# Optimization experiments

Measured on AMD Instinct MI355X. Metric: run time of the kernel, lower is better.

The kernel has to match this reference:

```python
import jax, jax.numpy as jnp
import numpy as np

T, D, E, K = 8192, 7168, 256, 8
G, LG = 8, 4  # n_expert_groups, n_limited_groups
ROUTE_SCALE = 2.5


def setup_inputs() -> dict:
    key = jax.random.key(0)
    k1, k2, k3 = jax.random.split(key, 3)
    x = jax.random.normal(k1, (T, D), dtype=jnp.float32)
    W = jax.random.normal(k2, (E, D), dtype=jnp.float32) * (1.0 / np.sqrt(D))
    bias = jax.random.normal(k3, (E,), dtype=jnp.float32) * 0.01
    return {"x": x, "W": W, "bias": bias}


def reference(x, W, bias):
    # linear scorer: [T, E]
    logits = jnp.einsum("td,ed->te", x, W)
    original_scores = jax.nn.sigmoid(logits)
    scores = original_scores + bias  # bias only affects routing, not weights

    # group selection: reshape [T, G, E//G]; group score = sum of top-2 (bias path)
    scores_g = scores.reshape(T, G, E // G)
    group_scores = jax.lax.top_k(scores_g, 2)[0].sum(axis=-1)  # [T, G]
    _, gidx = jax.lax.top_k(group_scores, LG)  # [T, LG]
    keep = jnp.any(jnp.arange(G)[None, None, :] == gidx[:, :, None], axis=1)  # [T, G]
    scores_masked = jnp.where(keep[:, :, None], scores_g, -jnp.inf).reshape(T, E)

    # final top-k experts
    _, indices = jax.lax.top_k(scores_masked, K)  # [T, K] int32
    weights = jnp.take_along_axis(original_scores, indices, axis=1)  # [T, K]
    weights = weights / weights.sum(axis=-1, keepdims=True)  # sigmoid normalization
    weights = weights * ROUTE_SCALE
    weights = weights.astype(x.dtype)

    # per-expert token counts (indices unique per row, so scatter(1)+sum == histogram)
    counts = jnp.zeros((E,), dtype=jnp.int32).at[indices.reshape(-1)].add(1)
    return weights, indices.astype(jnp.int64), counts
```

## Files before the change

### kernel.cpp

```cpp
#include <hip/hip_runtime.h>
#include <math.h>
#include <stdint.h>

#define T_TOK 8192
#define D_DIM 7168
#define E_EXP 256
#define K_SEL 8
#define G_GRP 8
#define LG_GRP 4
#define ROUTE_SCALE 2.5f

#define BM 64
#define BN 128
#define BK 64
#define NKT (D_DIM / BK)
#define SCALE_LO 2048.0f
#define INV_SCALE (1.0f / 2048.0f)

typedef _Float16 half_t;
typedef _Float16 half8 __attribute__((ext_vector_type(8)));
typedef float f32x4 __attribute__((ext_vector_type(4)));

#define WF_HALVES_PER_H (2 * 112 * 16 * 512)

__device__ __forceinline__ void load_lds16(const void* g, void* l) {
    __builtin_amdgcn_global_load_lds(
        (const __attribute__((address_space(1))) uint32_t*)g,
        (__attribute__((address_space(3))) uint32_t*)l, 16, 0, 0);
}

__global__ __launch_bounds__(256)
void convert_W_kernel(const float* __restrict__ W, half_t* __restrict__ Wf) {
    const int u = blockIdx.x * 256 + threadIdx.x;
    const int slot = u & 63;
    const int ks   = (u >> 6) & 1;
    const int p    = (u >> 7) & 7;
    const int t2   = u >> 10;
    const int kt   = t2 % 112;
    const int nb   = t2 / 112;
    const int e = nb * 128 + p * 16 + (slot & 15);
    const int k = kt * 64 + ks * 32 + (slot >> 4) * 8;

    const float* src = W + (size_t)e * D_DIM + k;
    float4 v0 = *(const float4*)src;
    float4 v1 = *(const float4*)(src + 4);
    float f[8] = {v0.x, v0.y, v0.z, v0.w, v1.x, v1.y, v1.z, v1.w};
    half8 hi, lo;
    #pragma unroll
    for (int j = 0; j < 8; j++) {
        const half_t h = (half_t)f[j];
        hi[j] = h;
        lo[j] = (half_t)((f[j] - (float)h) * SCALE_LO);
    }
    *(half8*)&Wf[(size_t)u * 8] = hi;
    *(half8*)&Wf[(size_t)WF_HALVES_PER_H + (size_t)u * 8] = lo;
}

__global__ __launch_bounds__(256, 3)
void gemm_logits_f16split(const float* __restrict__ x,
                          const half_t* __restrict__ Wf,
                          float* __restrict__ planes,
                          int nsplit) {
    __shared__ __align__(16) half_t Ah[4 * 2 * 64 * 8];
    __shared__ __align__(16) half_t Al[4 * 2 * 64 * 8];
    __shared__ __align__(16) half_t Bbuf[2][16][512];

    const int tid = threadIdx.x;
    const int bid = blockIdx.x;
    const int nmod  = 2 * nsplit;
    const int g     = bid % nmod;
    const int j     = bid / nmod;
    const int nb    = g & 1;
    const int split = g >> 1;
    const int row0 = j * BM;

    int ks0, kt_len;
    if (nsplit == 3) { ks0 = split * 38 - (split == 2 ? 1 : 0);
                       kt_len = split ? 37 : 38; }
    else             { ks0 = split * (NKT / nsplit);
                       kt_len = NKT / nsplit; }

    const float* __restrict__ xA = x + (size_t)row0 * D_DIM;
    float* __restrict__ plane = planes + (size_t)split * T_TOK * E_EXP;

    const int wave = tid >> 6, lane = tid & 63;
    const int q = lane >> 4;
    const int mp0 = (wave >> 1) * 2;
    const int np0 = (wave & 1) * 4;

    const half_t* __restrict__ wfl = Wf + ((size_t)(2 + nb) * 112) * 16 * 512
                                        + (size_t)lane * 8;

    float4 pa[2][2];

    auto load_A = [&](int kt) {
        const int kbase = kt * BK;
        #pragma unroll
        for (int i = 0; i < 2; i++) {
            const int u = i * 256 + tid;
            const int r = u >> 3, k8 = u & 7;
            const float* p = xA + (size_t)r * D_DIM + kbase + k8 * 8;
            pa[i][0] = *(const float4*)p;
            pa[i][1] = *(const float4*)(p + 4);
        }
    };

    auto stage_A = [&]() {
        #pragma unroll
        for (int i = 0; i < 2; i++) {
            const int u = i * 256 + tid;
            const int r = u >> 3, k8 = u & 7;
            float f[8] = {pa[i][0].x, pa[i][0].y, pa[i][0].z, pa[i][0].w,
                          pa[i][1].x, pa[i][1].y, pa[i][1].z, pa[i][1].w};
            half8 hi, lo;
            #pragma unroll
            for (int jj = 0; jj < 8; jj++) {
                const half_t h = (half_t)f[jj];
                hi[jj] = h;
                lo[jj] = (half_t)((f[jj] - (float)h) * SCALE_LO);
            }
            const int m = r & 15, qq = k8 & 3, kss = k8 >> 2;
            const int slot = (m + 16 * qq) ^ k8;
            const int off = (((r >> 4) * 2 + kss) * 64 + slot) * 8;
            *(half8*)&Ah[off] = hi;
            *(half8*)&Al[off] = lo;
        }
    };

    auto issue_B = [&](int tt) {
        const int kt = ks0 + tt;
        half_t* bb = &Bbuf[tt & 1][0][0];
        #pragma unroll
        for (int i = 0; i < 4; i++) {
            const int sl = i * 4 + wave;
            const half_t* src = Wf +
                ((size_t)(nb * 112 + kt) * 16 + sl) * 512 + lane * 8;
            load_lds16(src, bb + sl * 512);
        }
    };

    f32x4 ach[2][4] = {}, acc[2][4] = {};

    auto compute = [&](int tt, bool pref) {
        const int kt = ks0 + tt;
        const half_t* bb = &Bbuf[tt & 1][0][0];

        half8 bl[4][2];
        const size_t ktoff = (size_t)kt * (16 * 512);
        #pragma unroll
        for (int ni = 0; ni < 4; ni++)
            #pragma unroll
            for (int ks = 0; ks < 2; ks++) {
                const int s32 = (np0 + ni) * 2 + ks;
                bl[ni][ks] = *(const half8*)(wfl + ktoff + (size_t)s32 * 512);
            }
        if (pref) {
            issue_B(tt + 1);
            load_A(ks0 + tt + 1);
        }
        #pragma unroll
        for (int ks = 0; ks < 2; ks++) {
            const int slot = lane ^ ((ks << 2) | q);
            half8 ah[2], al[2], bh[4];
            #pragma unroll
            for (int mi = 0; mi < 2; mi++) {
                const int off = (((mp0 + mi) * 2 + ks) * 64 + slot) * 8;
                ah[mi] = *(const half8*)&Ah[off];
                al[mi] = *(const half8*)&Al[off];
            }
            #pragma unroll
            for (int ni = 0; ni < 4; ni++) {
                const int s32 = (np0 + ni) * 2 + ks;
                bh[ni] = *(const half8*)&bb[s32 * 512 + lane * 8];
            }
            #pragma unroll
            for (int mi = 0; mi < 2; mi++)
                #pragma unroll
                for (int ni = 0; ni < 4; ni++) {
                    ach[mi][ni] = __builtin_amdgcn_mfma_f32_16x16x32_f16(ah[mi], bh[ni], ach[mi][ni], 0, 0, 0);
                    acc[mi][ni] = __builtin_amdgcn_mfma_f32_16x16x32_f16(ah[mi], bl[ni][ks], acc[mi][ni], 0, 0, 0);
                    acc[mi][ni] = __builtin_amdgcn_mfma_f32_16x16x32_f16(al[mi], bh[ni], acc[mi][ni], 0, 0, 0);
                }
        }
    };

    issue_B(0);
    load_A(ks0);

    #pragma unroll 1
    for (int tt = 0; tt < kt_len; tt++) {
        __syncthreads();
        stage_A();
        __syncthreads();
        compute(tt, tt + 1 < kt_len);
    }

    const int col0 = nb * BN;
    #pragma unroll
    for (int mi = 0; mi < 2; mi++)
        #pragma unroll
        for (int ni = 0; ni < 4; ni++) {
            const f32x4 vh = ach[mi][ni];
            const f32x4 vc = acc[mi][ni];
            const int ex = col0 + (np0 + ni) * 16 + (lane & 15);
            #pragma unroll
            for (int r = 0; r < 4; r++) {
                const int tok = row0 + (mp0 + mi) * 16 + q * 4 + r;
                plane[(size_t)tok * E_EXP + ex] = vh[r] + vc[r] * INV_SCALE;
            }
        }
}

__global__ __launch_bounds__(256)
void routing_kernel(const float* __restrict__ planes,
                    const float* __restrict__ bias,
                    float* __restrict__ out_w,
                    float* __restrict__ out_i,
                    int nsplit) {
    const int wave = threadIdx.x >> 6;
    const int lane = threadIdx.x & 63;
    const int t    = blockIdx.x * 4 + wave;

    float lg[4] = {0.f, 0.f, 0.f, 0.f};
    for (int s = 0; s < nsplit; s++) {
        const float4 l = *(const float4*)(planes + (size_t)s * T_TOK * E_EXP +
                                          (size_t)t * E_EXP + lane * 4);
        lg[0] += l.x; lg[1] += l.y; lg[2] += l.z; lg[3] += l.w;
    }
    const float4 bi = *(const float4*)(bias + lane * 4);

    float orig[4], s[4];
    #pragma unroll
    for (int j = 0; j < 4; j++)
        orig[j] = 1.0f / (1.0f + expf(-lg[j]));
    s[0] = orig[0] + bi.x; s[1] = orig[1] + bi.y;
    s[2] = orig[2] + bi.z; s[3] = orig[3] + bi.w;

    float p1 = fmaxf(s[0], s[1]), p2 = fminf(s[0], s[1]);
    float q1 = fmaxf(s[2], s[3]), q2 = fminf(s[2], s[3]);
    float m1 = fmaxf(p1, q1);
    float m2 = fmaxf(fminf(p1, q1), (p1 >= q1) ? p2 : q2);

    #pragma unroll
    for (int off = 1; off <= 4; off <<= 1) {
        float o1 = __shfl_xor(m1, off);
        float o2 = __shfl_xor(m2, off);
        float M1 = fmaxf(m1, o1);
        float M2 = fmaxf(fminf(m1, o1), (m1 >= o1) ? m2 : o2);
        m1 = M1; m2 = M2;
    }
    const float gscore = m1 + m2;

    const int g = lane >> 3;
    int cnt = 0;
    #pragma unroll
    for (int j = 0; j < G_GRP; j++) {
        float gj = __shfl(gscore, j * 8);
        cnt += (gj > gscore || (gj == gscore && j < g)) ? 1 : 0;
    }
    const bool keep = (cnt < LG_GRP);

    float smask[4];
    #pragma unroll
    for (int j = 0; j < 4; j++) smask[j] = keep ? s[j] : -INFINITY;

    float wsum = 0.0f, my_o = 0.0f;
    int my_i = 0;

    #pragma unroll
    for (int k = 0; k < K_SEL; k++) {
        float bv = smask[0]; float bo = orig[0]; int bs = 0;
        if (smask[1] > bv) { bv = smask[1]; bo = orig[1]; bs = 1; }
        if (smask[2] > bv) { bv = smask[2]; bo = orig[2]; bs = 2; }
        if (smask[3] > bv) { bv = smask[3]; bo = orig[3]; bs = 3; }
        int bidx = lane * 4 + bs;

        #pragma unroll
        for (int off = 32; off >= 1; off >>= 1) {
            float ov = __shfl_xor(bv, off);
            float oo = __shfl_xor(bo, off);
            int   oi = __shfl_xor(bidx, off);
            if (ov > bv || (ov == bv && oi < bidx)) { bv = ov; bo = oo; bidx = oi; }
        }
        wsum += bo;
        if (lane == k) { my_o = bo; my_i = bidx; }
        if ((bidx >> 2) == lane) {
            const int sl = bidx & 3;
            smask[0] = (sl == 0) ? -INFINITY : smask[0];
            smask[1] = (sl == 1) ? -INFINITY : smask[1];
            smask[2] = (sl == 2) ? -INFINITY : smask[2];
            smask[3] = (sl == 3) ? -INFINITY : smask[3];
        }
    }

    if (lane < K_SEL) {
        out_w[(size_t)t * K_SEL + lane] = my_o * ROUTE_SCALE / wsum;
        out_i[(size_t)t * K_SEL + lane] = (float)my_i;
    }
}

__global__ __launch_bounds__(256)
void count_kernel(const float* __restrict__ idxf, float* __restrict__ out_c) {
    const float fe = (float)blockIdx.x;
    int c = 0;
    const float4* p = (const float4*)idxf;
    for (int i = threadIdx.x; i < (T_TOK * K_SEL / 4); i += 256) {
        float4 v = p[i];
        c += (v.x == fe) + (v.y == fe) + (v.z == fe) + (v.w == fe);
    }
    __shared__ int red[4];
    #pragma unroll
    for (int off = 32; off >= 1; off >>= 1) c += __shfl_down(c, off);
    if ((threadIdx.x & 63) == 0) red[threadIdx.x >> 6] = c;
    __syncthreads();
    if (threadIdx.x == 0)
        out_c[blockIdx.x] = (float)(red[0] + red[1] + red[2] + red[3]);
}

extern "C" void kernel_launch(void* const* d_in, const int* in_sizes, int n_in,
                              void* d_out, int out_size, void* d_ws, size_t ws_size,
                              hipStream_t stream) {
    const float* x    = (const float*)d_in[0];
    const float* W    = (const float*)d_in[1];
    const float* bias = (const float*)d_in[2];

    float* out   = (float*)d_out;
    float* out_w = out;
    float* out_i = out + (size_t)T_TOK * K_SEL;
    float* out_c = out + (size_t)2 * T_TOK * K_SEL;

    const size_t planeN  = (size_t)T_TOK * E_EXP;
    const size_t wfBytes = (size_t)2 * WF_HALVES_PER_H * sizeof(half_t);

    int nsplit = 3;
    if (ws_size != 0 && ws_size < 3 * planeN * sizeof(float) + wfBytes)
        nsplit = 2;
    const int grid = 128 * 2 * nsplit;

    float* planes = (float*)d_ws;
    half_t* Wf    = (half_t*)(planes + (size_t)nsplit * planeN);

    hipLaunchKernelGGL(convert_W_kernel, dim3(896), dim3(256), 0, stream, W, Wf);
    hipLaunchKernelGGL(gemm_logits_f16split, dim3(grid), dim3(256), 0, stream,
                       x, Wf, planes, nsplit);
    hipLaunchKernelGGL(routing_kernel, dim3(T_TOK / 4), dim3(256), 0, stream,
                       planes, bias, out_w, out_i, nsplit);
    hipLaunchKernelGGL(count_kernel, dim3(E_EXP), dim3(256), 0, stream,
                       out_i, out_c);
}
```

Before: 413.5 us.

## Widen GEMM tile to all experts, split K four ways, double-buffer A registers

Each GEMM block now covers all 256 expert columns (BN 256) instead of 128, so each x tile is loaded and split into hi/lo halves once rather than twice. The K dimension is split four ways, giving 512 blocks, and the prefetched A values alternate between two register sets so the next tile's global loads are in flight during compute. Barriers now wait with explicit vmcnt/lgkmcnt counts and sched_barrier fences. In exchange, occupancy drops to 2 blocks per CU, register and LDS use per block rise, and a fourth partial-sum plane must be written and read by the routing kernel.

```diff
diff --git a/kernel.cpp b/kernel.cpp
--- a/kernel.cpp
+++ b/kernel.cpp
@@ -11,7 +11,7 @@
 #define ROUTE_SCALE 2.5f
 
 #define BM 64
-#define BN 128
+#define BN 256
 #define BK 64
 #define NKT (D_DIM / BK)
 #define SCALE_LO 2048.0f
@@ -28,6 +28,15 @@
         (const __attribute__((address_space(1))) uint32_t*)g,
         (__attribute__((address_space(3))) uint32_t*)l, 16, 0, 0);
 }
+
+#define SYNC1() do { \
+    asm volatile("s_waitcnt vmcnt(4) lgkmcnt(0)" ::: "memory"); \
+    __builtin_amdgcn_sched_barrier(0); \
+    __builtin_amdgcn_s_barrier(); } while (0)
+#define SYNC2() do { \
+    asm volatile("s_waitcnt lgkmcnt(0)" ::: "memory"); \
+    __builtin_amdgcn_sched_barrier(0); \
+    __builtin_amdgcn_s_barrier(); } while (0)
 
 __global__ __launch_bounds__(256)
 void convert_W_kernel(const float* __restrict__ W, half_t* __restrict__ Wf) {
@@ -56,44 +65,44 @@
     *(half8*)&Wf[(size_t)WF_HALVES_PER_H + (size_t)u * 8] = lo;
 }
 
-__global__ __launch_bounds__(256, 3)
+__global__ __launch_bounds__(256, 2)
 void gemm_logits_f16split(const float* __restrict__ x,
                           const half_t* __restrict__ Wf,
                           float* __restrict__ planes,
                           int nsplit) {
     __shared__ __align__(16) half_t Ah[4 * 2 * 64 * 8];
     __shared__ __align__(16) half_t Al[4 * 2 * 64 * 8];
-    __shared__ __align__(16) half_t Bbuf[2][16][512];
+    __shared__ __align__(16) half_t Bbuf[2][32][512];
 
     const int tid = threadIdx.x;
     const int bid = blockIdx.x;
-    const int nmod  = 2 * nsplit;
-    const int g     = bid % nmod;
-    const int j     = bid / nmod;
-    const int nb    = g & 1;
-    const int split = g >> 1;
-    const int row0 = j * BM;
-
-    int ks0, kt_len;
-    if (nsplit == 3) { ks0 = split * 38 - (split == 2 ? 1 : 0);
-                       kt_len = split ? 37 : 38; }
-    else             { ks0 = split * (NKT / nsplit);
-                       kt_len = NKT / nsplit; }
+    int split, m_blk;
+    if (nsplit == 4) {
+        const int g = bid & 7;
+        split = g & 3;
+        m_blk = (g >> 2) * 64 + (bid >> 3);
+    } else {
+        split = bid & 1;
+        m_blk = bid >> 1;
+    }
+    const int kt_len = NKT / nsplit;
+    const int ks0    = split * kt_len;
+    const int row0   = m_blk * BM;
 
     const float* __restrict__ xA = x + (size_t)row0 * D_DIM;
     float* __restrict__ plane = planes + (size_t)split * T_TOK * E_EXP;
 
     const int wave = tid >> 6, lane = tid & 63;
     const int q = lane >> 4;
-    const int mp0 = (wave >> 1) * 2;
-    const int np0 = (wave & 1) * 4;
-
-    const half_t* __restrict__ wfl = Wf + ((size_t)(2 + nb) * 112) * 16 * 512
+    const int nbb = wave >> 1;
+    const int nlo = (wave & 1) * 4;
+
+    const half_t* __restrict__ wfl = Wf + ((size_t)(2 + nbb) * 112) * 16 * 512
                                         + (size_t)lane * 8;
 
-    float4 pa[2][2];
-
-    auto load_A = [&](int kt) {
+    float4 pa0[2][2], pa1[2][2];
+
+    auto load_A = [&](float4 (&pa)[2][2], int kt) {
         const int kbase = kt * BK;
         #pragma unroll
         for (int i = 0; i < 2; i++) {
@@ -105,7 +114,7 @@
         }
     };
 
-    auto stage_A = [&]() {
+    auto stage_A = [&](float4 (&pa)[2][2]) {
         #pragma unroll
         for (int i = 0; i < 2; i++) {
             const int u = i * 256 + tid;
@@ -127,54 +136,53 @@
         }
     };
 
-    auto issue_B = [&](int tt) {
-        const int kt = ks0 + tt;
-        half_t* bb = &Bbuf[tt & 1][0][0];
-        #pragma unroll
-        for (int i = 0; i < 4; i++) {
-            const int sl = i * 4 + wave;
+    auto issue_B = [&](int kt, int buf) {
+        half_t* bb = &Bbuf[buf][0][0];
+        #pragma unroll
+        for (int i = 0; i < 8; i++) {
+            const int s32 = i * 4 + wave;
+            const int nb2 = s32 >> 4, sl = s32 & 15;
             const half_t* src = Wf +
-                ((size_t)(nb * 112 + kt) * 16 + sl) * 512 + lane * 8;
-            load_lds16(src, bb + sl * 512);
+                ((size_t)(nb2 * 112 + kt) * 16 + sl) * 512 + lane * 8;
+            load_lds16(src, bb + s32 * 512);
         }
     };
 
-    f32x4 ach[2][4] = {}, acc[2][4] = {};
-
-    auto compute = [&](int tt, bool pref) {
-        const int kt = ks0 + tt;
+    f32x4 ach[4][4] = {}, acc[4][4] = {};
+
+    auto compute = [&](int tt, int ktB, float4 (&paN)[2][2], int ktA) {
         const half_t* bb = &Bbuf[tt & 1][0][0];
 
         half8 bl[4][2];
-        const size_t ktoff = (size_t)kt * (16 * 512);
+        const size_t ktoff = (size_t)(ks0 + tt) * (16 * 512);
         #pragma unroll
         for (int ni = 0; ni < 4; ni++)
             #pragma unroll
             for (int ks = 0; ks < 2; ks++) {
-                const int s32 = (np0 + ni) * 2 + ks;
-                bl[ni][ks] = *(const half8*)(wfl + ktoff + (size_t)s32 * 512);
-            }
-        if (pref) {
-            issue_B(tt + 1);
-            load_A(ks0 + tt + 1);
-        }
+                const int sl = (nlo + ni) * 2 + ks;
+                bl[ni][ks] = *(const half8*)(wfl + ktoff + (size_t)sl * 512);
+            }
+        __builtin_amdgcn_sched_barrier(0);
+        issue_B(ktB, (tt + 1) & 1);
+        __builtin_amdgcn_sched_barrier(0);
+        load_A(paN, ktA);
         #pragma unroll
         for (int ks = 0; ks < 2; ks++) {
             const int slot = lane ^ ((ks << 2) | q);
-            half8 ah[2], al[2], bh[4];
-            #pragma unroll
-            for (int mi = 0; mi < 2; mi++) {
-                const int off = (((mp0 + mi) * 2 + ks) * 64 + slot) * 8;
+            half8 ah[4], al[4], bh[4];
+            #pragma unroll
+            for (int mi = 0; mi < 4; mi++) {
+                const int off = ((mi * 2 + ks) * 64 + slot) * 8;
                 ah[mi] = *(const half8*)&Ah[off];
                 al[mi] = *(const half8*)&Al[off];
             }
             #pragma unroll
             for (int ni = 0; ni < 4; ni++) {
-                const int s32 = (np0 + ni) * 2 + ks;
+                const int s32 = ((wave * 4 + ni) * 2 + ks);
                 bh[ni] = *(const half8*)&bb[s32 * 512 + lane * 8];
             }
             #pragma unroll
-            for (int mi = 0; mi < 2; mi++)
+            for (int mi = 0; mi < 4; mi++)
                 #pragma unroll
                 for (int ni = 0; ni < 4; ni++) {
                     ach[mi][ni] = __builtin_amdgcn_mfma_f32_16x16x32_f16(ah[mi], bh[ni], ach[mi][ni], 0, 0, 0);
@@ -184,28 +192,43 @@
         }
     };
 
-    issue_B(0);
-    load_A(ks0);
-
+    load_A(pa0, ks0);
+    issue_B(ks0, 0);
+    load_A(pa1, ks0 + 1);
+
+    const int last = kt_len - 1;
     #pragma unroll 1
-    for (int tt = 0; tt < kt_len; tt++) {
-        __syncthreads();
-        stage_A();
-        __syncthreads();
-        compute(tt, tt + 1 < kt_len);
-    }
-
-    const int col0 = nb * BN;
-    #pragma unroll
-    for (int mi = 0; mi < 2; mi++)
+    for (int t2 = 0; t2 < kt_len; t2 += 2) {
+        {
+            const int tt = t2;
+            SYNC1();
+            stage_A(pa0);
+            SYNC2();
+            const int ktB = ks0 + (tt + 1 < kt_len ? tt + 1 : last);
+            const int ktA = ks0 + (tt + 2 < kt_len ? tt + 2 : last);
+            compute(tt, ktB, pa0, ktA);
+        }
+        {
+            const int tt = t2 + 1;
+            SYNC1();
+            stage_A(pa1);
+            SYNC2();
+            const int ktB = ks0 + (tt + 1 < kt_len ? tt + 1 : last);
+            const int ktA = ks0 + (tt + 2 < kt_len ? tt + 2 : last);
+            compute(tt, ktB, pa1, ktA);
+        }
+    }
+
+    #pragma unroll
+    for (int mi = 0; mi < 4; mi++)
         #pragma unroll
         for (int ni = 0; ni < 4; ni++) {
             const f32x4 vh = ach[mi][ni];
             const f32x4 vc = acc[mi][ni];
-            const int ex = col0 + (np0 + ni) * 16 + (lane & 15);
+            const int ex = (wave * 4 + ni) * 16 + (lane & 15);
             #pragma unroll
             for (int r = 0; r < 4; r++) {
-                const int tok = row0 + (mp0 + mi) * 16 + q * 4 + r;
+                const int tok = row0 + mi * 16 + q * 4 + r;
                 plane[(size_t)tok * E_EXP + ex] = vh[r] + vc[r] * INV_SCALE;
             }
         }
@@ -332,10 +355,10 @@
     const size_t planeN  = (size_t)T_TOK * E_EXP;
     const size_t wfBytes = (size_t)2 * WF_HALVES_PER_H * sizeof(half_t);
 
-    int nsplit = 3;
-    if (ws_size != 0 && ws_size < 3 * planeN * sizeof(float) + wfBytes)
+    int nsplit = 4;
+    if (ws_size != 0 && ws_size < 4 * planeN * sizeof(float) + wfBytes)
         nsplit = 2;
-    const int grid = 128 * 2 * nsplit;
+    const int grid = 128 * nsplit;
 
     float* planes = (float*)d_ws;
     half_t* Wf    = (half_t*)(planes + (size_t)nsplit * planeN);
```

Result: slower. 519.1 us (+25.6%).

## Double-buffer A register prefetch two tiles ahead with partial vmcnt waits

Applied to the files above, without the earlier changes.

Splits the A-tile register prefetch into two ping-pong register sets so x loads are issued two k-tiles ahead, and unrolls the main loop by two to alternate them. The __syncthreads calls are replaced with explicit s_waitcnt vmcnt(4)/lgkmcnt(0) plus s_barrier, so the newest global loads may stay in flight across the barrier. Sched barriers pin the order of the LDS-direct B issue and the A loads. The tail clamps indices to the last tile and issues redundant loads unconditionally. This raises register pressure and relies on hand-counted vmcnt values being correct.

```diff
diff --git a/kernel.cpp b/kernel.cpp
--- a/kernel.cpp
+++ b/kernel.cpp
@@ -28,6 +28,17 @@
         (const __attribute__((address_space(1))) uint32_t*)g,
         (__attribute__((address_space(3))) uint32_t*)l, 16, 0, 0);
 }
+
+#define SYNC1() do { \
+    asm volatile("s_waitcnt vmcnt(4) lgkmcnt(0)" ::: "memory"); \
+    __builtin_amdgcn_sched_barrier(0); \
+    __builtin_amdgcn_s_barrier(); \
+    __builtin_amdgcn_sched_barrier(0); } while (0)
+#define SYNC2() do { \
+    asm volatile("s_waitcnt lgkmcnt(0)" ::: "memory"); \
+    __builtin_amdgcn_sched_barrier(0); \
+    __builtin_amdgcn_s_barrier(); \
+    __builtin_amdgcn_sched_barrier(0); } while (0)
 
 __global__ __launch_bounds__(256)
 void convert_W_kernel(const float* __restrict__ W, half_t* __restrict__ Wf) {
@@ -91,9 +102,9 @@
     const half_t* __restrict__ wfl = Wf + ((size_t)(2 + nb) * 112) * 16 * 512
                                         + (size_t)lane * 8;
 
-    float4 pa[2][2];
-
-    auto load_A = [&](int kt) {
+    float4 pa0[2][2], pa1[2][2];
+
+    auto load_A = [&](float4 (&pa)[2][2], int kt) {
         const int kbase = kt * BK;
         #pragma unroll
         for (int i = 0; i < 2; i++) {
@@ -105,7 +116,7 @@
         }
     };
 
-    auto stage_A = [&]() {
+    auto stage_A = [&](float4 (&pa)[2][2]) {
         #pragma unroll
         for (int i = 0; i < 2; i++) {
             const int u = i * 256 + tid;
@@ -127,9 +138,8 @@
         }
     };
 
-    auto issue_B = [&](int tt) {
-        const int kt = ks0 + tt;
-        half_t* bb = &Bbuf[tt & 1][0][0];
+    auto issue_B = [&](int kt, int buf) {
+        half_t* bb = &Bbuf[buf][0][0];
         #pragma unroll
         for (int i = 0; i < 4; i++) {
             const int sl = i * 4 + wave;
@@ -141,23 +151,22 @@
 
     f32x4 ach[2][4] = {}, acc[2][4] = {};
 
-    auto compute = [&](int tt, bool pref) {
-        const int kt = ks0 + tt;
+    auto compute = [&](int tt, int ktB, float4 (&paN)[2][2], int ktA) {
         const half_t* bb = &Bbuf[tt & 1][0][0];
 
         half8 bl[4][2];
-        const size_t ktoff = (size_t)kt * (16 * 512);
+        const size_t ktoff = (size_t)(ks0 + tt) * (16 * 512);
         #pragma unroll
         for (int ni = 0; ni < 4; ni++)
             #pragma unroll
             for (int ks = 0; ks < 2; ks++) {
-                const int s32 = (np0 + ni) * 2 + ks;
-                bl[ni][ks] = *(const half8*)(wfl + ktoff + (size_t)s32 * 512);
-            }
-        if (pref) {
-            issue_B(tt + 1);
-            load_A(ks0 + tt + 1);
-        }
+                const int sl = (np0 + ni) * 2 + ks;
+                bl[ni][ks] = *(const half8*)(wfl + ktoff + (size_t)sl * 512);
+            }
+        __builtin_amdgcn_sched_barrier(0);
+        issue_B(ktB, (tt + 1) & 1);
+        __builtin_amdgcn_sched_barrier(0);
+        load_A(paN, ktA);
         #pragma unroll
         for (int ks = 0; ks < 2; ks++) {
             const int slot = lane ^ ((ks << 2) | q);
@@ -184,15 +193,32 @@
         }
     };
 
-    issue_B(0);
-    load_A(ks0);
-
+    load_A(pa0, ks0);
+    issue_B(ks0, 0);
+    load_A(pa1, ks0 + 1);
+
+    const int last = kt_len - 1;
+    int tt = 0;
     #pragma unroll 1
-    for (int tt = 0; tt < kt_len; tt++) {
-        __syncthreads();
-        stage_A();
-        __syncthreads();
-        compute(tt, tt + 1 < kt_len);
+    while (true) {
+        {
+            SYNC1();
+            stage_A(pa0);
+            SYNC2();
+            const int ktB = ks0 + (tt + 1 < kt_len ? tt + 1 : last);
+            const int ktA = ks0 + (tt + 2 < kt_len ? tt + 2 : last);
+            compute(tt, ktB, pa0, ktA);
+        }
+        if (++tt == kt_len) break;
+        {
+            SYNC1();
+            stage_A(pa1);
+            SYNC2();
+            const int ktB = ks0 + (tt + 1 < kt_len ? tt + 1 : last);
+            const int ktA = ks0 + (tt + 2 < kt_len ? tt + 2 : last);
+            compute(tt, ktB, pa1, ktA);
+        }
+        if (++tt == kt_len) break;
     }
 
     const int col0 = nb * BN;
```

Measured after the change: 704.5 us. 1.7x slower.
